# Kernel tuning notes

Hardware: AMD Instinct MI355X
Metric: run time of the kernel (lower is better)

## Reference

```python
import jax, jax.numpy as jnp
import numpy as np

# Dims (match init_kwargs / input_specs)
B, S, HID = 1, 2048, 2048
NH, NKV, HD = 16, 4, 128          # head_dim = HID // NH
REP = NH // NKV                    # num_key_value_groups
BLOCK_SIZE, LOCAL_BLOCKS, SINK_NUM = 8, 4, 4
SCALING = HD ** -0.5


def rotate_half(x):
    x1, x2 = jnp.split(x, 2, axis=-1)
    return jnp.concatenate([-x2, x1], axis=-1)


def setup_inputs() -> dict:
    key = jax.random.key(0)
    ks = jax.random.split(key, 7)
    return {
        "hidden_states": jax.random.normal(ks[0], (B, S, HID), jnp.float32),
        "cos": jax.random.uniform(ks[1], (B, S, HD), jnp.float32, minval=-1.0, maxval=1.0),
        "sin": jax.random.uniform(ks[2], (B, S, HD), jnp.float32, minval=-1.0, maxval=1.0),
        # Projection weights stored as [in, out] so x @ W matches nn.Linear (bias=False).
        "Wq": 0.02 * jax.random.normal(ks[3], (HID, NH * HD), jnp.float32),
        "Wk": 0.02 * jax.random.normal(ks[4], (HID, NKV * HD), jnp.float32),
        "Wv": 0.02 * jax.random.normal(ks[5], (HID, NKV * HD), jnp.float32),
        "Wo": 0.02 * jax.random.normal(ks[6], (NH * HD, HID), jnp.float32),
    }


def sink_local_mask(seq_len):
    # query i attends to: sink tokens j < min(SINK_NUM, i), and local window
    # max(0, i - LOCAL_BLOCKS*BLOCK_SIZE) <= j <= i (diagonal included so every
    # row has at least one valid key; see notes).
    i = jnp.arange(seq_len)[:, None]
    j = jnp.arange(seq_len)[None, :]
    sink = j < jnp.minimum(SINK_NUM, i)
    local = (j >= i - LOCAL_BLOCKS * BLOCK_SIZE) & (j <= i)
    return sink | local  # [S, S] bool, broadcast over (B, H)


def reference(hidden_states, cos, sin, Wq, Wk, Wv, Wo):
    # projections -> [B, H, S, D]
    q = (hidden_states @ Wq).reshape(B, S, NH, HD).transpose(0, 2, 1, 3)
    k = (hidden_states @ Wk).reshape(B, S, NKV, HD).transpose(0, 2, 1, 3)
    v = (hidden_states @ Wv).reshape(B, S, NKV, HD).transpose(0, 2, 1, 3)
    # rotary embedding, cos/sin broadcast over head dim (unsqueeze_dim=1)
    c = cos[:, None, :, :]
    s = sin[:, None, :, :]
    q = q * c + rotate_half(q) * s
    k = k * c + rotate_half(k) * s
    # repeat_kv (GQA) -> [B, NH, S, D]
    k = jnp.repeat(k, REP, axis=1)
    v = jnp.repeat(v, REP, axis=1)
    # sink + local sparse attention (dense compute + mask, as in source)
    scores = jnp.einsum('bhqd,bhkd->bhqk', q, k) * SCALING
    mask = sink_local_mask(S)
    scores = jnp.where(mask, scores, -jnp.inf)
    attn_weights = jax.nn.softmax(scores, axis=-1)
    attn_output = jnp.einsum('bhqk,bhkd->bhqd', attn_weights, v)
    # Faithful to source: view(B, S, -1) on the [B, H, S, D] layout WITHOUT a
    # transpose(1,2) first (the original code omits it).
    attn_output = attn_output.reshape(B, S, NH * HD)
    attn_output = attn_output @ Wo
    return attn_output, attn_weights
```

## Files before the change

### kernel.cpp

```cpp
#include <hip/hip_runtime.h>

typedef unsigned short ushort_t;
typedef __attribute__((ext_vector_type(8))) short short8;
typedef __attribute__((ext_vector_type(4))) float f32x4;
typedef __attribute__((ext_vector_type(8))) unsigned short us8;
typedef __attribute__((ext_vector_type(4))) unsigned short us4;

#define SEQ 2048
#define HIDD 2048
#define XLD 3072
#define SCALING 0.08838834764831843f

__device__ __forceinline__ float bf2f(ushort_t u) {
    unsigned int x = ((unsigned int)u) << 16;
    return __builtin_bit_cast(float, x);
}
__device__ __forceinline__ ushort_t f2bf(float f) {
    unsigned int u = __builtin_bit_cast(unsigned int, f);
    u += 0x7fffu + ((u >> 16) & 1u);
    return (ushort_t)(u >> 16);
}

__device__ __forceinline__ void transpose_tile(
    const float* __restrict__ W, ushort_t* __restrict__ Wt,
    int N, int n0, int k0, int dstRow0) {
    __shared__ ushort_t t[64 * 80];
    const int tid = threadIdx.x;
    {
        const int kl = tid >> 4;
        const int nc = (tid & 15) * 4;
        #pragma unroll
        for (int p = 0; p < 4; ++p) {
            int k = kl + p * 16;
            float4 v = *(const float4*)(W + (size_t)(k0 + k) * N + n0 + nc);
            t[(nc + 0) * 80 + k] = f2bf(v.x);
            t[(nc + 1) * 80 + k] = f2bf(v.y);
            t[(nc + 2) * 80 + k] = f2bf(v.z);
            t[(nc + 3) * 80 + k] = f2bf(v.w);
        }
    }
    __syncthreads();
    {
        const int nl = tid >> 3;
        const int kc = (tid & 7) * 8;
        #pragma unroll
        for (int p = 0; p < 2; ++p) {
            int n = nl + p * 32;
            *(us8*)(Wt + (size_t)(dstRow0 + n) * HIDD + k0 + kc) =
                *(const us8*)&t[n * 80 + kc];
        }
    }
}

__global__ __launch_bounds__(256) void transpose_all(
    const float* __restrict__ Wq, const float* __restrict__ Wk,
    const float* __restrict__ Wv, const float* __restrict__ Wo,
    const float* __restrict__ hid,
    ushort_t* __restrict__ Wqkvt, ushort_t* __restrict__ Wot,
    ushort_t* __restrict__ Hb) {
    int bx = blockIdx.x, k0 = blockIdx.y * 64;
    if (bx < 32)       transpose_tile(Wq, Wqkvt, 2048, bx * 64,        k0, bx * 64);
    else if (bx < 40)  transpose_tile(Wk, Wqkvt, 512,  (bx - 32) * 64, k0, 2048 + (bx - 32) * 64);
    else if (bx < 48)  transpose_tile(Wv, Wqkvt, 512,  (bx - 40) * 64, k0, 2560 + (bx - 40) * 64);
    else if (bx < 80)  transpose_tile(Wo, Wot,   2048, (bx - 48) * 64, k0, (bx - 48) * 64);
    else {
        int chunk = (bx - 80) * 32 + blockIdx.y;
        size_t base = (size_t)chunk * 4096 + threadIdx.x * 16;
        #pragma unroll
        for (int p = 0; p < 4; ++p) {
            float4 v = *(const float4*)(hid + base + p * 4);
            us4 o;
            o[0] = f2bf(v.x); o[1] = f2bf(v.y); o[2] = f2bf(v.z); o[3] = f2bf(v.w);
            *(us4*)(Hb + base + p * 4) = o;
        }
    }
}

__global__ __launch_bounds__(256) void gemm_splitk(
    const ushort_t* __restrict__ A, int lda,
    const ushort_t* __restrict__ Bt, int ldb,
    ushort_t* __restrict__ P, int ldc,
    const int4 kexts) {
    __shared__ ushort_t lA[2 * 128 * 32];
    __shared__ ushort_t lB[2 * 128 * 32];
    const int tid = threadIdx.x;
    const int wave = tid >> 6, lane = tid & 63;
    const int wm = wave >> 1, wn = wave & 1;
    const int quad = lane >> 4, l16 = lane & 15;
    const int m0 = blockIdx.y * 128, n0 = blockIdx.x * 128;
    const int z = blockIdx.z;

    const int ke[4] = {kexts.x, kexts.y, kexts.z, kexts.w};
    int koff = 0;
    for (int zz = 0; zz < 4; ++zz) if (zz < z) koff += ke[zz];
    const int kext = ke[z];

    A  += (size_t)koff;
    Bt += (size_t)koff;
    P  += (size_t)z * ((size_t)gridDim.y * 128) * ldc;

    const int srow = lane >> 2;
    const int scol = 8 * ((lane & 3) ^ (srow & 3));

    f32x4 acc[4][4] = {};

    const ushort_t* Ab = A  + (size_t)(m0 + wave * 16 + srow) * lda + scol;
    const ushort_t* Bb = Bt + (size_t)(n0 + wave * 16 + srow) * ldb + scol;
    ushort_t* lAw = lA + (wave * 16) * 32;
    ushort_t* lBw = lB + (wave * 16) * 32;

    const int rsw = (quad ^ (l16 & 3)) * 8;

    for (int kk = 0; kk < kext; kk += 64) {
        __syncthreads();
        #pragma unroll
        for (int kh = 0; kh < 2; ++kh) {
            #pragma unroll
            for (int c = 0; c < 2; ++c) {
                __builtin_amdgcn_global_load_lds(
                    (const __attribute__((address_space(1))) unsigned int*)(const void*)
                        (Ab + (size_t)(c * 64) * lda + kk + kh * 32),
                    (__attribute__((address_space(3))) unsigned int*)(void*)
                        (lAw + kh * 128 * 32 + c * 64 * 32), 16, 0, 0);
                __builtin_amdgcn_global_load_lds(
                    (const __attribute__((address_space(1))) unsigned int*)(const void*)
                        (Bb + (size_t)(c * 64) * ldb + kk + kh * 32),
                    (__attribute__((address_space(3))) unsigned int*)(void*)
                        (lBw + kh * 128 * 32 + c * 64 * 32), 16, 0, 0);
            }
        }
        __syncthreads();
        #pragma unroll
        for (int kh = 0; kh < 2; ++kh) {
            short8 af[4], bfr[4];
            #pragma unroll
            for (int mt = 0; mt < 4; ++mt)
                af[mt] = *(const short8*)&lA[kh * 128 * 32 + (wm * 64 + mt * 16 + l16) * 32 + rsw];
            #pragma unroll
            for (int nt = 0; nt < 4; ++nt)
                bfr[nt] = *(const short8*)&lB[kh * 128 * 32 + (wn * 64 + nt * 16 + l16) * 32 + rsw];
            #pragma unroll
            for (int mt = 0; mt < 4; ++mt) {
                #pragma unroll
                for (int nt = 0; nt < 4; ++nt)
                    acc[mt][nt] = __builtin_amdgcn_mfma_f32_16x16x32_bf16(
                        af[mt], bfr[nt], acc[mt][nt], 0, 0, 0);
            }
        }
    }

    #pragma unroll
    for (int mt = 0; mt < 4; ++mt) {
        #pragma unroll
        for (int nt = 0; nt < 4; ++nt) {
            int gm = m0 + wm * 64 + mt * 16 + quad * 4;
            int gn = n0 + wn * 64 + nt * 16 + l16;
            #pragma unroll
            for (int r = 0; r < 4; ++r)
                P[(size_t)(gm + r) * ldc + gn] = f2bf(acc[mt][nt][r]);
        }
    }
}

#define RWAVES (SEQ * 10)
#define VWAVES (SEQ * 2)
__global__ __launch_bounds__(256) void reduce_x(
    const ushort_t* __restrict__ P, ushort_t* __restrict__ X,
    const float* __restrict__ cosp, const float* __restrict__ sinp) {
    const size_t ZS = (size_t)SEQ * XLD;
    int wbase = (blockIdx.x * 4 + (threadIdx.x >> 6)) * 4;
    int lane = threadIdx.x & 63;
    #pragma unroll
    for (int pp = 0; pp < 4; ++pp) {
        int wid = wbase + pp;
        if (wid < RWAVES) {
            int s = wid / 10, seg = wid % 10;
            int c0 = seg * 256 + lane * 4;
            size_t base = (size_t)s * XLD + c0;
            us4 a = *(const us4*)(P + base);
            us4 b = *(const us4*)(P + ZS + base);
            float x[4];
            #pragma unroll
            for (int t = 0; t < 4; ++t) x[t] = bf2f(a[t]) + bf2f(b[t]);
            float p[4];
            #pragma unroll
            for (int t = 0; t < 4; ++t) p[t] = __shfl_xor(x[t], 16, 64);
            int d = (lane * 4) & 127;
            float4 cv = *(const float4*)(cosp + (size_t)s * 128 + d);
            float4 sv = *(const float4*)(sinp + (size_t)s * 128 + d);
            float sgn = (lane & 16) ? 1.f : -1.f;
            us4 o;
            o[0] = f2bf(x[0] * cv.x + sgn * p[0] * sv.x);
            o[1] = f2bf(x[1] * cv.y + sgn * p[1] * sv.y);
            o[2] = f2bf(x[2] * cv.z + sgn * p[2] * sv.z);
            o[3] = f2bf(x[3] * cv.w + sgn * p[3] * sv.w);
            *(us4*)(X + base) = o;
        } else {
            int w2 = wid - RWAVES;
            int s = w2 >> 1;
            int c0 = 2560 + (w2 & 1) * 256 + lane * 4;
            size_t base = (size_t)s * XLD + c0;
            us4 a = *(const us4*)(P + base);
            us4 b = *(const us4*)(P + ZS + base);
            us4 o;
            #pragma unroll
            for (int t = 0; t < 4; ++t) o[t] = f2bf(bf2f(a[t]) + bf2f(b[t]));
            *(us4*)(X + base) = o;
        }
    }
}

__global__ __launch_bounds__(256) void reduce_out3(
    const ushort_t* __restrict__ P, float* __restrict__ out) {
    const size_t ZS = (size_t)SEQ * HIDD;
    size_t idx0 = ((size_t)blockIdx.x * 256 + threadIdx.x) * 16;
    #pragma unroll
    for (int pp = 0; pp < 4; ++pp) {
        size_t idx = idx0 + pp * 4;
        us4 a = *(const us4*)(P + idx);
        us4 b = *(const us4*)(P + ZS + idx);
        us4 c = *(const us4*)(P + 2 * ZS + idx);
        f32x4 o;
        o[0] = bf2f(a[0]) + bf2f(b[0]) + bf2f(c[0]);
        o[1] = bf2f(a[1]) + bf2f(b[1]) + bf2f(c[1]);
        o[2] = bf2f(a[2]) + bf2f(b[2]) + bf2f(c[2]);
        o[3] = bf2f(a[3]) + bf2f(b[3]) + bf2f(c[3]);
        __builtin_nontemporal_store(o, (f32x4*)(out + idx));
    }
}

#define SMLD 136
__device__ __forceinline__ float qk_round_lds(
    const char* __restrict__ smb, const float* qf,
    int jg, int dg, int lo, int nsink, int w0, int r) {
    int jj = r * 16 + jg;
    int row;
    if (jj < nsink) row = 48 + jj;
    else {
        int widx = lo + jj - nsink - w0;
        if (widx > 47) widx = 47;
        row = widx;
    }
    const char* base = smb + row * 272 + ((dg * 64) ^ ((row & 3) << 6));
    float p = 0.f;
    #pragma unroll
    for (int pq = 0; pq < 4; ++pq) {
        us8 v = *(const us8*)(base + pq * 16);
        #pragma unroll
        for (int t = 0; t < 8; ++t) p += qf[pq * 8 + t] * bf2f(v[t]);
    }
    p += __shfl_xor(p, 1, 64);
    p += __shfl_xor(p, 2, 64);
    return p * SCALING;
}

__global__ __launch_bounds__(256) void attn_kernel(
    const ushort_t* __restrict__ X, float* __restrict__ Wts,
    ushort_t* __restrict__ Aout) {
    __shared__ ushort_t sm[104 * SMLD];
    char* smb = (char*)sm;
    const int tid = threadIdx.x;
    const int lane = tid & 63;
    const int wv = tid >> 6;
    const int h = blockIdx.x >> 7;
    const int i0 = (blockIdx.x & 127) << 4;
    const int w0 = (i0 >= 32) ? (i0 - 32) : 0;
    const int kvh = h >> 2;

    const ushort_t* Kg = X + 2048 + kvh * 128;
    const ushort_t* Vg = X + 2560 + kvh * 128;

    #pragma unroll
    for (int p = 0; p < 7; ++p) {
        int tau = p * 16 + (tid >> 4);
        if (tau < 104) {
            int rr = (tau < 52) ? tau : (tau - 52);
            int grow = (rr < 48) ? (w0 + rr) : (rr - 48);
            const ushort_t* src = ((tau < 52) ? Kg : Vg) + (size_t)grow * XLD + (tid & 15) * 8;
            int dst = tau * 272 + (((tid & 15) * 16) ^ ((tau & 3) << 6));
            *(us8*)(smb + dst) = *(const us8*)src;
        }
    }
    __syncthreads();

    const int dg = lane & 3;
    const int jg = lane >> 2;

    for (int ii = 0; ii < 4; ++ii) {
        const int i = i0 + wv * 4 + ii;

        float qf[32];
        {
            const ushort_t* Q = X + (size_t)i * XLD + h * 128 + dg * 32;
            #pragma unroll
            for (int pq = 0; pq < 4; ++pq) {
                us8 v = *(const us8*)(Q + pq * 8);
                #pragma unroll
                for (int t = 0; t < 8; ++t) qf[pq * 8 + t] = bf2f(v[t]);
            }
        }

        int lo = i - 32; if (lo < 0) lo = 0;
        int nsink = lo < 4 ? lo : 4;
        int NJ = nsink + (i - lo + 1);

        float s0 = qk_round_lds(smb, qf, jg, dg, lo, nsink, w0, 0);
        float s1 = qk_round_lds(smb, qf, jg, dg, lo, nsink, w0, 1);
        float s2 = qk_round_lds(smb, qf, jg, dg, lo, nsink, w0, 2);

        int src = (lane & 15) * 4;
        float m0 = __shfl(s0, src, 64);
        float m1 = __shfl(s1, src, 64);
        float m2 = __shfl(s2, src, 64);
        float mysc = (lane < 16) ? m0 : ((lane < 32) ? m1 : m2);
        if (lane >= NJ) mysc = -1e30f;

        float m = mysc;
        #pragma unroll
        for (int off = 32; off > 0; off >>= 1) m = fmaxf(m, __shfl_xor(m, off, 64));

        float e = (lane < NJ) ? expf(mysc - m) : 0.f;
        float l = e;
        #pragma unroll
        for (int off = 32; off > 0; off >>= 1) l += __shfl_xor(l, off, 64);
        float w = e / l;

        float* row = Wts + ((size_t)h * SEQ + i) * SEQ;
        #pragma unroll
        for (int s = 0; s < 8; ++s) {
            f32x4 o;
            #pragma unroll
            for (int t = 0; t < 4; ++t) {
                int c = s * 256 + lane * 4 + t;
                bool in = (c < nsink) || (c >= lo && c <= i);
                int jjc = in ? ((c < nsink) ? c : (nsink + c - lo)) : 0;
                float wv2 = __shfl(w, jjc, 64);
                o[t] = in ? wv2 : 0.f;
            }
            __builtin_nontemporal_store(o, (f32x4*)(row + s * 256 + lane * 4));
        }

        float o0 = 0.f, o1 = 0.f;
        for (int jj = 0; jj < NJ; ++jj) {
            int vrow;
            if (jj < nsink) vrow = 100 + jj;
            else {
                int widx = lo + jj - nsink - w0;
                vrow = 52 + widx;
            }
            float pb = __shfl(w, jj, 64);
            unsigned int vv = *(const unsigned int*)
                (smb + vrow * 272 + ((4 * lane) ^ ((vrow & 3) << 6)));
            o0 += pb * bf2f((ushort_t)(vv & 0xffff));
            o1 += pb * bf2f((ushort_t)(vv >> 16));
        }
        int r = h * 128 + (i >> 4);
        int c = (i & 15) * 128 + 2 * lane;
        ushort_t* Ar = Aout + (size_t)r * HIDD + c;
        Ar[0] = f2bf(o0);
        Ar[1] = f2bf(o1);
    }
}

extern "C" void kernel_launch(void* const* d_in, const int* in_sizes, int n_in,
                              void* d_out, int out_size, void* d_ws, size_t ws_size,
                              hipStream_t stream) {
    if (n_in < 7) return;
    const float* hid  = (const float*)d_in[0];
    const float* cosp = (const float*)d_in[1];
    const float* sinp = (const float*)d_in[2];
    const float* Wq   = (const float*)d_in[3];
    const float* Wk   = (const float*)d_in[4];
    const float* Wv   = (const float*)d_in[5];
    const float* Wo   = (const float*)d_in[6];

    float* out = (float*)d_out;
    float* wts = out + (size_t)SEQ * HIDD;

    ushort_t* Hb    = (ushort_t*)d_ws;
    ushort_t* Wqkvt = Hb    + (size_t)2048 * 2048;
    ushort_t* Wot   = Wqkvt + (size_t)3072 * 2048;
    ushort_t* X     = Wot   + (size_t)2048 * 2048;
    ushort_t* Am    = X     + (size_t)SEQ * XLD;
    ushort_t* Pqkv  = Am    + (size_t)SEQ * HIDD;
    ushort_t* Pout  = Pqkv  + 2 * (size_t)SEQ * XLD;
    size_t need = ((char*)(Pout + 3 * (size_t)SEQ * HIDD)) - (char*)d_ws;
    if (ws_size < need) return;

    dim3 blk(256);
    transpose_all<<<dim3(112, 32), blk, 0, stream>>>(
        Wq, Wk, Wv, Wo, hid, Wqkvt, Wot, Hb);

    gemm_splitk<<<dim3(24, 16, 2), blk, 0, stream>>>(
        Hb, HIDD, Wqkvt, 2048, Pqkv, XLD, make_int4(1024, 1024, 0, 0));
    reduce_x<<<(RWAVES + VWAVES) / 16, blk, 0, stream>>>(
        Pqkv, X, cosp, sinp);

    attn_kernel<<<SEQ * 16 / 16, blk, 0, stream>>>(X, wts, Am);

    gemm_splitk<<<dim3(16, 16, 3), blk, 0, stream>>>(
        Am, HIDD, Wot, 2048, Pout, HIDD, make_int4(704, 704, 640, 0));
    reduce_out3<<<(SEQ * HIDD) / (256 * 16), blk, 0, stream>>>(Pout, out);
}
```

Baseline: 450.5 us.

## Enlarge GEMM tiles to 256x256 with double-buffered LDS prefetch and tile swizzle

The split-K GEMM now uses 512-thread blocks computing 256x256 tiles, with two LDS stages so the next K tile loads while MFMAs run on the current one. Tile indices are remapped so neighbouring blocks share data in cache. The output projection moves to 4-way split-K with an updated reduction kernel. The aim is more operand reuse and hidden load latency, at the cost of fewer blocks, which may underfill the CUs, and one extra partial buffer to reduce.

```diff
diff --git a/kernel.cpp b/kernel.cpp
--- a/kernel.cpp
+++ b/kernel.cpp
@@ -76,84 +76,109 @@
     }
 }
 
-__global__ __launch_bounds__(256) void gemm_splitk(
+#define GLL16(s, d) __builtin_amdgcn_global_load_lds( \
+    (const __attribute__((address_space(1))) unsigned int*)(const void*)(s), \
+    (__attribute__((address_space(3))) unsigned int*)(void*)(d), 16, 0, 0)
+
+__global__ __launch_bounds__(512, 2) void gemm_splitk(
     const ushort_t* __restrict__ A, int lda,
     const ushort_t* __restrict__ Bt, int ldb,
     ushort_t* __restrict__ P, int ldc,
     const int4 kexts) {
-    __shared__ ushort_t lA[2 * 128 * 32];
-    __shared__ ushort_t lB[2 * 128 * 32];
+    __shared__ ushort_t lA[2 * 2 * 256 * 32];
+    __shared__ ushort_t lB[2 * 2 * 256 * 32];
     const int tid = threadIdx.x;
     const int wave = tid >> 6, lane = tid & 63;
-    const int wm = wave >> 1, wn = wave & 1;
+    const int wm = wave >> 2, wn = wave & 3;
     const int quad = lane >> 4, l16 = lane & 15;
-    const int m0 = blockIdx.y * 128, n0 = blockIdx.x * 128;
     const int z = blockIdx.z;
+
+    const int T = gridDim.x * gridDim.y;
+    const int t0 = blockIdx.y * gridDim.x + blockIdx.x;
+    const int ts = (t0 & 7) * (T >> 3) + (t0 >> 3);
+    const int m0 = (ts / gridDim.x) * 256;
+    const int n0 = (ts % gridDim.x) * 256;
 
     const int ke[4] = {kexts.x, kexts.y, kexts.z, kexts.w};
     int koff = 0;
     for (int zz = 0; zz < 4; ++zz) if (zz < z) koff += ke[zz];
     const int kext = ke[z];
+    const int NT = kext >> 6;
 
     A  += (size_t)koff;
     Bt += (size_t)koff;
-    P  += (size_t)z * ((size_t)gridDim.y * 128) * ldc;
-
-    const int srow = lane >> 2;
-    const int scol = 8 * ((lane & 3) ^ (srow & 3));
-
-    f32x4 acc[4][4] = {};
-
-    const ushort_t* Ab = A  + (size_t)(m0 + wave * 16 + srow) * lda + scol;
-    const ushort_t* Bb = Bt + (size_t)(n0 + wave * 16 + srow) * ldb + scol;
-    ushort_t* lAw = lA + (wave * 16) * 32;
-    ushort_t* lBw = lB + (wave * 16) * 32;
-
-    const int rsw = (quad ^ (l16 & 3)) * 8;
-
-    for (int kk = 0; kk < kext; kk += 64) {
-        __syncthreads();
+    P  += (size_t)z * ((size_t)gridDim.y * 256) * ldc;
+
+    const int srow = tid >> 2;
+    const int scb  = tid & 3;
+    const int scol = 8 * (scb ^ (srow & 3));
+    const int rsw  = (quad ^ (l16 & 3)) * 8;
+
+    const ushort_t* Ab = A  + (size_t)(m0 + srow) * lda + scol;
+    const ushort_t* Bb = Bt + (size_t)(n0 + srow) * ldb + scol;
+    ushort_t* ldst = lA + srow * 32 + scb * 8;
+    ushort_t* ldstB = lB + srow * 32 + scb * 8;
+
+    f32x4 acc[8][4] = {};
+
+    auto STAGE = [&](int t, int b) {
+        const int kk = t * 64;
         #pragma unroll
         for (int kh = 0; kh < 2; ++kh) {
             #pragma unroll
-            for (int c = 0; c < 2; ++c) {
-                __builtin_amdgcn_global_load_lds(
-                    (const __attribute__((address_space(1))) unsigned int*)(const void*)
-                        (Ab + (size_t)(c * 64) * lda + kk + kh * 32),
-                    (__attribute__((address_space(3))) unsigned int*)(void*)
-                        (lAw + kh * 128 * 32 + c * 64 * 32), 16, 0, 0);
-                __builtin_amdgcn_global_load_lds(
-                    (const __attribute__((address_space(1))) unsigned int*)(const void*)
-                        (Bb + (size_t)(c * 64) * ldb + kk + kh * 32),
-                    (__attribute__((address_space(3))) unsigned int*)(void*)
-                        (lBw + kh * 128 * 32 + c * 64 * 32), 16, 0, 0);
+            for (int rr = 0; rr < 2; ++rr) {
+                GLL16(Ab + (size_t)(rr * 128) * lda + kk + kh * 32,
+                      ldst + b * 16384 + kh * 8192 + rr * 128 * 32);
+                GLL16(Bb + (size_t)(rr * 128) * ldb + kk + kh * 32,
+                      ldstB + b * 16384 + kh * 8192 + rr * 128 * 32);
             }
         }
-        __syncthreads();
+    };
+
+    STAGE(0, 0);
+    STAGE(1, 1);
+    asm volatile("s_waitcnt vmcnt(8)" ::: "memory");
+    __builtin_amdgcn_s_barrier();
+    __builtin_amdgcn_sched_barrier(0);
+
+    for (int t = 0; t < NT; ++t) {
+        const int b = t & 1;
         #pragma unroll
         for (int kh = 0; kh < 2; ++kh) {
-            short8 af[4], bfr[4];
-            #pragma unroll
-            for (int mt = 0; mt < 4; ++mt)
-                af[mt] = *(const short8*)&lA[kh * 128 * 32 + (wm * 64 + mt * 16 + l16) * 32 + rsw];
+            short8 af[8], bfr[4];
+            #pragma unroll
+            for (int mt = 0; mt < 8; ++mt)
+                af[mt] = *(const short8*)
+                    &lA[b * 16384 + kh * 8192 + (wm * 128 + mt * 16 + l16) * 32 + rsw];
             #pragma unroll
             for (int nt = 0; nt < 4; ++nt)
-                bfr[nt] = *(const short8*)&lB[kh * 128 * 32 + (wn * 64 + nt * 16 + l16) * 32 + rsw];
-            #pragma unroll
-            for (int mt = 0; mt < 4; ++mt) {
+                bfr[nt] = *(const short8*)
+                    &lB[b * 16384 + kh * 8192 + (wn * 64 + nt * 16 + l16) * 32 + rsw];
+            #pragma unroll
+            for (int mt = 0; mt < 8; ++mt)
                 #pragma unroll
                 for (int nt = 0; nt < 4; ++nt)
                     acc[mt][nt] = __builtin_amdgcn_mfma_f32_16x16x32_bf16(
                         af[mt], bfr[nt], acc[mt][nt], 0, 0, 0);
-            }
-        }
+        }
+        __builtin_amdgcn_sched_barrier(0);
+        __builtin_amdgcn_s_barrier();
+        __builtin_amdgcn_sched_barrier(0);
+        if (t + 2 < NT) {
+            STAGE(t + 2, b);
+            asm volatile("s_waitcnt vmcnt(8)" ::: "memory");
+        } else {
+            asm volatile("s_waitcnt vmcnt(0)" ::: "memory");
+        }
+        __builtin_amdgcn_s_barrier();
+        __builtin_amdgcn_sched_barrier(0);
     }
 
     #pragma unroll
-    for (int mt = 0; mt < 4; ++mt) {
+    for (int mt = 0; mt < 8; ++mt) {
         #pragma unroll
         for (int nt = 0; nt < 4; ++nt) {
-            int gm = m0 + wm * 64 + mt * 16 + quad * 4;
+            int gm = m0 + wm * 128 + mt * 16 + quad * 4;
             int gn = n0 + wn * 64 + nt * 16 + l16;
             #pragma unroll
             for (int r = 0; r < 4; ++r)
@@ -210,7 +235,7 @@
     }
 }
 
-__global__ __launch_bounds__(256) void reduce_out3(
+__global__ __launch_bounds__(256) void reduce_out4(
     const ushort_t* __restrict__ P, float* __restrict__ out) {
     const size_t ZS = (size_t)SEQ * HIDD;
     size_t idx0 = ((size_t)blockIdx.x * 256 + threadIdx.x) * 16;
@@ -220,11 +245,12 @@
         us4 a = *(const us4*)(P + idx);
         us4 b = *(const us4*)(P + ZS + idx);
         us4 c = *(const us4*)(P + 2 * ZS + idx);
+        us4 d = *(const us4*)(P + 3 * ZS + idx);
         f32x4 o;
-        o[0] = bf2f(a[0]) + bf2f(b[0]) + bf2f(c[0]);
-        o[1] = bf2f(a[1]) + bf2f(b[1]) + bf2f(c[1]);
-        o[2] = bf2f(a[2]) + bf2f(b[2]) + bf2f(c[2]);
-        o[3] = bf2f(a[3]) + bf2f(b[3]) + bf2f(c[3]);
+        o[0] = (bf2f(a[0]) + bf2f(b[0])) + (bf2f(c[0]) + bf2f(d[0]));
+        o[1] = (bf2f(a[1]) + bf2f(b[1])) + (bf2f(c[1]) + bf2f(d[1]));
+        o[2] = (bf2f(a[2]) + bf2f(b[2])) + (bf2f(c[2]) + bf2f(d[2]));
+        o[3] = (bf2f(a[3]) + bf2f(b[3])) + (bf2f(c[3]) + bf2f(d[3]));
         __builtin_nontemporal_store(o, (f32x4*)(out + idx));
     }
 }
@@ -384,21 +410,21 @@
     ushort_t* Am    = X     + (size_t)SEQ * XLD;
     ushort_t* Pqkv  = Am    + (size_t)SEQ * HIDD;
     ushort_t* Pout  = Pqkv  + 2 * (size_t)SEQ * XLD;
-    size_t need = ((char*)(Pout + 3 * (size_t)SEQ * HIDD)) - (char*)d_ws;
+    size_t need = ((char*)(Pout + 4 * (size_t)SEQ * HIDD)) - (char*)d_ws;
     if (ws_size < need) return;
 
     dim3 blk(256);
     transpose_all<<<dim3(112, 32), blk, 0, stream>>>(
         Wq, Wk, Wv, Wo, hid, Wqkvt, Wot, Hb);
 
-    gemm_splitk<<<dim3(24, 16, 2), blk, 0, stream>>>(
+    gemm_splitk<<<dim3(12, 8, 2), dim3(512), 0, stream>>>(
         Hb, HIDD, Wqkvt, 2048, Pqkv, XLD, make_int4(1024, 1024, 0, 0));
     reduce_x<<<(RWAVES + VWAVES) / 16, blk, 0, stream>>>(
         Pqkv, X, cosp, sinp);
 
     attn_kernel<<<SEQ * 16 / 16, blk, 0, stream>>>(X, wts, Am);
 
-    gemm_splitk<<<dim3(16, 16, 3), blk, 0, stream>>>(
-        Am, HIDD, Wot, 2048, Pout, HIDD, make_int4(704, 704, 640, 0));
-    reduce_out3<<<(SEQ * HIDD) / (256 * 16), blk, 0, stream>>>(Pout, out);
-}
+    gemm_splitk<<<dim3(8, 8, 4), dim3(512), 0, stream>>>(
+        Am, HIDD, Wot, 2048, Pout, HIDD, make_int4(512, 512, 512, 512));
+    reduce_out4<<<(SEQ * HIDD) / (256 * 16), blk, 0, stream>>>(Pout, out);
+}
```

Measured after the change: 465.4 us. +3.3%, slower.
